# Performance work log

Measured on AMD Instinct MI355X. Metric: run time of the kernel, lower is better.

The kernel has to match this reference:

```python
import jax, jax.numpy as jnp
import numpy as np

N = 50000        # nodes
E_RAND = 800000  # random edges (avg degree 16)
F_IN = 512       # num_features
H = 128          # h_dim * num_heads = 16 * 8
C = 40           # num_classes
NEG_SLOPE = 0.2  # GATv2 default


def _glorot(key, shape):
    lim = float(np.sqrt(6.0 / (shape[0] + shape[1])))
    return jax.random.uniform(key, shape, jnp.float32, -lim, lim)


def setup_inputs() -> dict:
    key = jax.random.key(0)
    ks = jax.random.split(key, 12)
    src = jax.random.randint(ks[0], (E_RAND,), 0, N)
    dst = jax.random.randint(ks[1], (E_RAND,), 0, N)
    loop = jnp.arange(N)  # self-loops (GATv2Conv add_self_loops=True)
    edge_index = jnp.stack([jnp.concatenate([src, loop]),
                            jnp.concatenate([dst, loop])]).astype(jnp.int32)
    x = jax.random.normal(ks[2], (N, F_IN), jnp.float32)
    return {
        "x": x,
        "edge_index": edge_index,
        "W1l": _glorot(ks[3], (F_IN, H)), "b1l": jnp.zeros((H,), jnp.float32),
        "W1r": _glorot(ks[4], (F_IN, H)), "b1r": jnp.zeros((H,), jnp.float32),
        "a1": _glorot(ks[5], (H, 1)).reshape(H),
        "bias1": jnp.zeros((H,), jnp.float32),
        "W2l": _glorot(ks[6], (H, C)), "b2l": jnp.zeros((C,), jnp.float32),
        "W2r": _glorot(ks[7], (H, C)), "b2r": jnp.zeros((C,), jnp.float32),
        "a2": _glorot(ks[8], (C, 1)).reshape(C),
        "bias2": jnp.zeros((C,), jnp.float32),
    }


def gatv2_layer(x, src, dst, Wl, bl, Wr, br, att, bias, n):
    # PyG GATv2Conv, heads=1: xl = lin_l(x) (source side), xr = lin_r(x) (target side)
    xl = x @ Wl + bl                                   # [N, C_out]
    xr = x @ Wr + br                                   # [N, C_out]
    # edge score e_ij = a^T LeakyReLU(xl[j] + xr[i])
    e = jax.nn.leaky_relu(xl[src] + xr[dst], negative_slope=NEG_SLOPE) @ att  # [E]
    # segment softmax over edges grouped by destination node
    m = jax.ops.segment_max(e, dst, num_segments=n)    # every node has a self-loop
    ex = jnp.exp(e - m[dst])
    den = jax.ops.segment_sum(ex, dst, num_segments=n)
    alpha = ex / den[dst]                              # [E]
    # weighted scatter-aggregate of source-transformed features
    out = jax.ops.segment_sum(alpha[:, None] * xl[src], dst, num_segments=n)
    return out + bias


def reference(x, edge_index, W1l, b1l, W1r, b1r, a1, bias1,
              W2l, b2l, W2r, b2r, a2, bias2):
    # eval mode: dropout(p=0.6) is identity
    src, dst = edge_index[0], edge_index[1]
    n = x.shape[0]
    h = gatv2_layer(x, src, dst, W1l, b1l, W1r, b1r, a1, bias1, n)
    h = jax.nn.elu(h)
    h = gatv2_layer(h, src, dst, W2l, b2l, W2r, b2r, a2, bias2, n)
    return (h, jax.nn.log_softmax(h, axis=1))
```

## Files before the change

kernel.cpp:

```cpp
#include <hip/hip_runtime.h>
#include <math.h>

#define FIN 512
#define H1 128
#define C2 40
#define C2P 64

typedef __attribute__((ext_vector_type(8))) short short8;
typedef __attribute__((ext_vector_type(4))) float f32x4;

__device__ __forceinline__ ushort f2bf(float f) {
    union { float f; unsigned u; } c; c.f = f;
    unsigned u = c.u;
    return (ushort)((u + 0x7fffu + ((u >> 16) & 1u)) >> 16);
}
__device__ __forceinline__ float bf2f_lo(unsigned u) { return __uint_as_float(u << 16); }
__device__ __forceinline__ float bf2f_hi(unsigned u) { return __uint_as_float(u & 0xffff0000u); }

__global__ void count_k(const int* __restrict__ dst, int* __restrict__ cnt, int E) {
    int e = blockIdx.x * 256 + threadIdx.x;
    if (e < E) atomicAdd(&cnt[dst[e] + 1], 1);
}

__global__ __launch_bounds__(1024) void scan_k(int* __restrict__ arr, int ntot) {
    __shared__ int part[1024];
    int t = threadIdx.x;
    int chunk = (((ntot + 1023) / 1024) + 3) & ~3;
    int b = t * chunk;
    int s = 0;
    bool full = (b + chunk <= ntot);
    if (full) {
#pragma unroll 4
        for (int j = 0; j < chunk; j += 4) {
            int4 v = *reinterpret_cast<const int4*>(&arr[b + j]);
            s += v.x + v.y + v.z + v.w;
        }
    } else {
        for (int j = b; j < ntot; j++) s += arr[j];
    }
    part[t] = s;
    __syncthreads();
    for (int off = 1; off < 1024; off <<= 1) {
        int v = (t >= off) ? part[t - off] : 0;
        __syncthreads();
        part[t] += v;
        __syncthreads();
    }
    int run = (t == 0) ? 0 : part[t - 1];
    if (full) {
        for (int j = 0; j < chunk; j += 4) {
            int4 v = *reinterpret_cast<const int4*>(&arr[b + j]);
            int r0 = run + v.x, r1 = r0 + v.y, r2 = r1 + v.z, r3 = r2 + v.w;
            *reinterpret_cast<int4*>(&arr[b + j]) = make_int4(r0, r1, r2, r3);
            run = r3;
        }
    } else {
        for (int j = b; j < ntot; j++) { run += arr[j]; arr[j] = run; }
    }
}

__global__ void fill_k(const int* __restrict__ src, const int* __restrict__ dst,
                       const int* __restrict__ rowptr, int* __restrict__ fillp,
                       int* __restrict__ csr, int E) {
    int e = blockIdx.x * 256 + threadIdx.x;
    if (e < E) {
        int d = dst[e];
        int p = atomicAdd(&fillp[d], 1);
        csr[rowptr[d] + p] = src[e];
    }
}

__global__ void prep_k(const float* __restrict__ W1l, const float* __restrict__ W1r,
                       ushort* __restrict__ Wt2) {
    int idx = blockIdx.x * 256 + threadIdx.x;
    int kc  = idx >> 11;
    int rem = idx & 2047;
    int col = rem >> 3;
    int j   = rem & 7;
    int k   = kc * 8 + j;
    float v = (col < H1) ? W1l[k * H1 + col] : W1r[k * H1 + (col - H1)];
    Wt2[idx] = f2bf(v);
}

__global__ void prep2_k(const float* __restrict__ W2l, const float* __restrict__ W2r,
                        ushort* __restrict__ Ws) {
    int idx = blockIdx.x * 256 + threadIdx.x;
    if (idx >= 80 * H1) return;
    int col = idx >> 7;
    int k   = idx & 127;
    float v = (col < C2) ? W2l[k * C2 + col] : W2r[k * C2 + (col - C2)];
    Ws[idx] = f2bf(v);
}

__global__ __launch_bounds__(256) void gemm1_k(
    const float* __restrict__ x, const ushort* __restrict__ Wt2,
    const float* __restrict__ bl, const float* __restrict__ br,
    ushort* __restrict__ xlb, float* __restrict__ xr, int n)
{
    __shared__ ushort As[64][40];
    __shared__ ushort Bs[256][36];

    const int tid = threadIdx.x;
    const int r0  = blockIdx.x * 64;
    const int w    = tid >> 6;
    const int lane = tid & 63;
    const int l15  = lane & 15;
    const int lhi  = lane >> 4;

    f32x4 acc[4][4];
#pragma unroll
    for (int m = 0; m < 4; m++)
#pragma unroll
        for (int nn = 0; nn < 4; nn++) acc[m][nn] = (f32x4){0.f, 0.f, 0.f, 0.f};

    const int arow = tid >> 2;
    const int akc  = (tid & 3) * 8;
    const int arow_g = min(r0 + arow, n - 1);
    const float* aptr = x + (size_t)arow_g * FIN + akc;

    for (int kk = 0; kk < FIN; kk += 32) {
        float4 v0 = *reinterpret_cast<const float4*>(aptr + kk);
        float4 v1 = *reinterpret_cast<const float4*>(aptr + kk + 4);
        short8 ah;
        ah[0] = (short)f2bf(v0.x); ah[1] = (short)f2bf(v0.y);
        ah[2] = (short)f2bf(v0.z); ah[3] = (short)f2bf(v0.w);
        ah[4] = (short)f2bf(v1.x); ah[5] = (short)f2bf(v1.y);
        ah[6] = (short)f2bf(v1.z); ah[7] = (short)f2bf(v1.w);
        *reinterpret_cast<short8*>(&As[arow][akc]) = ah;

        int kc0 = kk >> 3;
#pragma unroll
        for (int q = 0; q < 4; q++) {
            short8 bh = *reinterpret_cast<const short8*>(&Wt2[(size_t)((kc0 + q) * 256 + tid) * 8]);
            *reinterpret_cast<short8*>(&Bs[tid][q * 8]) = bh;
        }
        __syncthreads();

        short8 af[4], bfr[4];
#pragma unroll
        for (int m = 0; m < 4; m++)
            af[m] = *reinterpret_cast<const short8*>(&As[m * 16 + l15][lhi * 8]);
#pragma unroll
        for (int nn = 0; nn < 4; nn++)
            bfr[nn] = *reinterpret_cast<const short8*>(&Bs[w * 64 + nn * 16 + l15][lhi * 8]);
#pragma unroll
        for (int m = 0; m < 4; m++)
#pragma unroll
            for (int nn = 0; nn < 4; nn++)
                acc[m][nn] = __builtin_amdgcn_mfma_f32_16x16x32_bf16(af[m], bfr[nn], acc[m][nn], 0, 0, 0);
        __syncthreads();
    }

#pragma unroll
    for (int nn = 0; nn < 4; nn++) {
        int col = w * 64 + nn * 16 + l15;
        bool left = (col < H1);
        float bias = left ? bl[col] : br[col - H1];
#pragma unroll
        for (int m = 0; m < 4; m++) {
#pragma unroll
            for (int r = 0; r < 4; r++) {
                int row = r0 + m * 16 + lhi * 4 + r;
                if (row < n) {
                    float v = acc[m][nn][r] + bias;
                    if (left) xlb[(size_t)row * H1 + col] = f2bf(v);
                    else      xr [(size_t)row * H1 + (col - H1)] = v;
                }
            }
        }
    }
}

__global__ __launch_bounds__(256) void edge1_k(
    const ushort* __restrict__ xlb, const float* xr,
    const int* __restrict__ rowptr, const int* __restrict__ csr,
    const float* __restrict__ att, const float* __restrict__ bias,
    float* h, int n)
{
    int wid  = threadIdx.x >> 6;
    int lane = threadIdx.x & 63;
    int grp  = lane >> 4;
    int gl   = lane & 15;
    int i = blockIdx.x * 4 + wid;
    if (i >= n) return;

    const float* xrp = &xr[(size_t)i * H1 + gl * 8];
    float4 xr0 = *reinterpret_cast<const float4*>(xrp);
    float4 xr1v = *reinterpret_cast<const float4*>(xrp + 4);
    float xrv[8] = {xr0.x, xr0.y, xr0.z, xr0.w, xr1v.x, xr1v.y, xr1v.z, xr1v.w};
    float4 a0 = *reinterpret_cast<const float4*>(&att[gl * 8]);
    float4 a1 = *reinterpret_cast<const float4*>(&att[gl * 8 + 4]);
    float av[8] = {a0.x, a0.y, a0.z, a0.w, a1.x, a1.y, a1.z, a1.w};

    int e0 = rowptr[i], e1 = rowptr[i + 1];

    float m = -INFINITY, den = 0.f;
    float acc[8];
#pragma unroll
    for (int f = 0; f < 8; f++) acc[f] = 0.f;

    int e = e0 + grp;
    uint4 u;
    if (e < e1) {
        int s = csr[e];
        u = *reinterpret_cast<const uint4*>(&xlb[(size_t)s * H1 + gl * 8]);
    }
    while (e < e1) {
        uint4 cu = u;
        int en = e + 4;
        if (en < e1) {
            int s2 = csr[en];
            u = *reinterpret_cast<const uint4*>(&xlb[(size_t)s2 * H1 + gl * 8]);
        }
        float xlv[8];
        xlv[0] = bf2f_lo(cu.x); xlv[1] = bf2f_hi(cu.x);
        xlv[2] = bf2f_lo(cu.y); xlv[3] = bf2f_hi(cu.y);
        xlv[4] = bf2f_lo(cu.z); xlv[5] = bf2f_hi(cu.z);
        xlv[6] = bf2f_lo(cu.w); xlv[7] = bf2f_hi(cu.w);
        float p = 0.f;
#pragma unroll
        for (int f = 0; f < 8; f++) {
            float t = xlv[f] + xrv[f];
            t = t > 0.f ? t : 0.2f * t;
            p += t * av[f];
        }
#pragma unroll
        for (int o = 8; o > 0; o >>= 1) p += __shfl_xor(p, o);
        float mn = fmaxf(m, p);
        float sc = __expf(m - mn);
        float wgt = __expf(p - mn);
        den = den * sc + wgt;
#pragma unroll
        for (int f = 0; f < 8; f++) acc[f] = acc[f] * sc + wgt * xlv[f];
        m = mn;
        e = en;
    }

    float mstar = m;
    mstar = fmaxf(mstar, __shfl_xor(mstar, 16));
    mstar = fmaxf(mstar, __shfl_xor(mstar, 32));
    float scale = __expf(m - mstar);
    den *= scale;
#pragma unroll
    for (int f = 0; f < 8; f++) acc[f] *= scale;
    den += __shfl_xor(den, 16); den += __shfl_xor(den, 32);
#pragma unroll
    for (int f = 0; f < 8; f++) {
        acc[f] += __shfl_xor(acc[f], 16);
        acc[f] += __shfl_xor(acc[f], 32);
    }

    if (grp == 0) {
        float inv = 1.f / den;
        float o[8];
#pragma unroll
        for (int f = 0; f < 8; f++) {
            float v = acc[f] * inv + bias[gl * 8 + f];
            o[f] = v > 0.f ? v : expm1f(v);
        }
        float* hp = &h[(size_t)i * H1 + gl * 8];
        *reinterpret_cast<float4*>(hp)     = make_float4(o[0], o[1], o[2], o[3]);
        *reinterpret_cast<float4*>(hp + 4) = make_float4(o[4], o[5], o[6], o[7]);
    }
}

__global__ __launch_bounds__(256) void gemm2_k(
    const float* __restrict__ h, const ushort* __restrict__ Ws,
    const float* __restrict__ bl, const float* __restrict__ br,
    ushort* __restrict__ xl2b, float* __restrict__ xr2, int n)
{
    __shared__ ushort WsL[80][136];

    const int tid = threadIdx.x;
    const int w    = tid >> 6;
    const int lane = tid & 63;
    const int l15  = lane & 15;
    const int lhi  = lane >> 4;
    const int r0 = blockIdx.x * 64;

#pragma unroll
    for (int q = 0; q < 5; q++) {
        int c = tid + q * 256;
        int col = c >> 4;
        int k0  = (c & 15) * 8;
        *reinterpret_cast<short8*>(&WsL[col][k0]) =
            *reinterpret_cast<const short8*>(&Ws[col * H1 + k0]);
    }
    __syncthreads();

    const int arow = min(r0 + w * 16 + l15, n - 1);
    const float* ap = &h[(size_t)arow * H1 + lhi * 8];

    f32x4 acc[5];
#pragma unroll
    for (int nt = 0; nt < 5; nt++) acc[nt] = (f32x4){0.f, 0.f, 0.f, 0.f};

#pragma unroll
    for (int kc = 0; kc < 4; kc++) {
        float4 v0 = *reinterpret_cast<const float4*>(ap + kc * 32);
        float4 v1 = *reinterpret_cast<const float4*>(ap + kc * 32 + 4);
        short8 af;
        af[0] = (short)f2bf(v0.x); af[1] = (short)f2bf(v0.y);
        af[2] = (short)f2bf(v0.z); af[3] = (short)f2bf(v0.w);
        af[4] = (short)f2bf(v1.x); af[5] = (short)f2bf(v1.y);
        af[6] = (short)f2bf(v1.z); af[7] = (short)f2bf(v1.w);
#pragma unroll
        for (int nt = 0; nt < 5; nt++) {
            short8 bf = *reinterpret_cast<const short8*>(&WsL[nt * 16 + l15][kc * 32 + lhi * 8]);
            acc[nt] = __builtin_amdgcn_mfma_f32_16x16x32_bf16(af, bf, acc[nt], 0, 0, 0);
        }
    }

#pragma unroll
    for (int nt = 0; nt < 5; nt++) {
        int col = nt * 16 + l15;
        float bias = (col < C2) ? bl[col] : br[col - C2];
#pragma unroll
        for (int r = 0; r < 4; r++) {
            int row = r0 + w * 16 + lhi * 4 + r;
            if (row < n) {
                float v = acc[nt][r] + bias;
                if (col < C2) xl2b[(size_t)row * C2P + col] = f2bf(v);
                else          xr2 [(size_t)row * C2  + (col - C2)] = v;
            }
        }
    }
    {
        int row = r0 + w * 16 + l15;
        int part = lhi;
        if (part < 3 && row < n) {
            uint4 z = make_uint4(0u, 0u, 0u, 0u);
            *reinterpret_cast<uint4*>(&xl2b[(size_t)row * C2P + C2 + part * 8]) = z;
        }
    }
}

__global__ __launch_bounds__(256) void edge2_k(
    const ushort* __restrict__ xl2b, const float* __restrict__ xr2,
    const int* __restrict__ rowptr, const int* __restrict__ csr,
    const float* __restrict__ att, const float* __restrict__ bias,
    float* __restrict__ out, int n)
{
    int wid  = threadIdx.x >> 6;
    int lane = threadIdx.x & 63;
    int grp  = lane >> 3;
    int gl   = lane & 7;
    int i = blockIdx.x * 4 + wid;
    if (i >= n) return;

    float xrv[8], av[8];
#pragma unroll
    for (int f = 0; f < 8; f++) {
        int idx = gl * 8 + f;
        bool real = idx < C2;
        xrv[f] = real ? xr2[(size_t)i * C2 + idx] : 0.f;
        av[f]  = real ? att[idx] : 0.f;
    }

    int e0 = rowptr[i], e1 = rowptr[i + 1];

    float m = -INFINITY, den = 0.f;
    float acc[8];
#pragma unroll
    for (int f = 0; f < 8; f++) acc[f] = 0.f;

    int e = e0 + grp;
    uint4 u;
    if (e < e1) {
        int s = csr[e];
        u = *reinterpret_cast<const uint4*>(&xl2b[(size_t)s * C2P + gl * 8]);
    }
    while (e < e1) {
        uint4 cu = u;
        int en = e + 8;
        if (en < e1) {
            int s2 = csr[en];
            u = *reinterpret_cast<const uint4*>(&xl2b[(size_t)s2 * C2P + gl * 8]);
        }
        float xlv[8];
        xlv[0] = bf2f_lo(cu.x); xlv[1] = bf2f_hi(cu.x);
        xlv[2] = bf2f_lo(cu.y); xlv[3] = bf2f_hi(cu.y);
        xlv[4] = bf2f_lo(cu.z); xlv[5] = bf2f_hi(cu.z);
        xlv[6] = bf2f_lo(cu.w); xlv[7] = bf2f_hi(cu.w);
        float p = 0.f;
#pragma unroll
        for (int f = 0; f < 8; f++) {
            float t = xlv[f] + xrv[f];
            t = t > 0.f ? t : 0.2f * t;
            p += t * av[f];
        }
#pragma unroll
        for (int o = 4; o > 0; o >>= 1) p += __shfl_xor(p, o);
        float mn = fmaxf(m, p);
        float sc = __expf(m - mn);
        float wgt = __expf(p - mn);
        den = den * sc + wgt;
#pragma unroll
        for (int f = 0; f < 8; f++) acc[f] = acc[f] * sc + wgt * xlv[f];
        m = mn;
        e = en;
    }

    float mstar = m;
    mstar = fmaxf(mstar, __shfl_xor(mstar, 8));
    mstar = fmaxf(mstar, __shfl_xor(mstar, 16));
    mstar = fmaxf(mstar, __shfl_xor(mstar, 32));
    float scale = __expf(m - mstar);
    den *= scale;
#pragma unroll
    for (int f = 0; f < 8; f++) acc[f] *= scale;
    den += __shfl_xor(den, 8); den += __shfl_xor(den, 16); den += __shfl_xor(den, 32);
#pragma unroll
    for (int f = 0; f < 8; f++) {
        acc[f] += __shfl_xor(acc[f], 8);
        acc[f] += __shfl_xor(acc[f], 16);
        acc[f] += __shfl_xor(acc[f], 32);
    }

    float inv = 1.f / den;
    bool real_lane = gl < 5;
    float o[8];
#pragma unroll
    for (int f = 0; f < 8; f++) {
        int idx = gl * 8 + f;
        o[f] = acc[f] * inv + (idx < C2 ? bias[idx] : 0.f);
    }

    float mv = -INFINITY;
    if (real_lane) {
#pragma unroll
        for (int f = 0; f < 8; f++) mv = fmaxf(mv, o[f]);
    }
    mv = fmaxf(mv, __shfl_xor(mv, 1));
    mv = fmaxf(mv, __shfl_xor(mv, 2));
    mv = fmaxf(mv, __shfl_xor(mv, 4));
    float se = 0.f;
    if (real_lane) {
#pragma unroll
        for (int f = 0; f < 8; f++) se += __expf(o[f] - mv);
    }
    se += __shfl_xor(se, 1); se += __shfl_xor(se, 2); se += __shfl_xor(se, 4);
    float lse = mv + logf(se);

    if (grp == 0 && real_lane) {
        float* op = &out[(size_t)i * C2 + gl * 8];
        *reinterpret_cast<float4*>(op)     = make_float4(o[0], o[1], o[2], o[3]);
        *reinterpret_cast<float4*>(op + 4) = make_float4(o[4], o[5], o[6], o[7]);
        float* lp = &out[(size_t)n * C2 + (size_t)i * C2 + gl * 8];
        *reinterpret_cast<float4*>(lp)     = make_float4(o[0] - lse, o[1] - lse, o[2] - lse, o[3] - lse);
        *reinterpret_cast<float4*>(lp + 4) = make_float4(o[4] - lse, o[5] - lse, o[6] - lse, o[7] - lse);
    }
}

extern "C" void kernel_launch(void* const* d_in, const int* in_sizes, int n_in,
                              void* d_out, int out_size, void* d_ws, size_t ws_size,
                              hipStream_t stream) {
    const float* x    = (const float*)d_in[0];
    const int*   ei   = (const int*)  d_in[1];
    const float* W1l  = (const float*)d_in[2];
    const float* b1l  = (const float*)d_in[3];
    const float* W1r  = (const float*)d_in[4];
    const float* b1r  = (const float*)d_in[5];
    const float* a1   = (const float*)d_in[6];
    const float* bias1= (const float*)d_in[7];
    const float* W2l  = (const float*)d_in[8];
    const float* b2l  = (const float*)d_in[9];
    const float* W2r  = (const float*)d_in[10];
    const float* b2r  = (const float*)d_in[11];
    const float* a2   = (const float*)d_in[12];
    const float* bias2= (const float*)d_in[13];

    const int N = in_sizes[0] / FIN;
    const int E = in_sizes[1] / 2;
    const int* src = ei;
    const int* dst = ei + E;

    float*  xr1 = (float*)d_ws;
    float*  xr2 = xr1 + (size_t)N * H1;
    ushort* xlb = (ushort*)(xr2 + (size_t)N * C2);
    ushort* xl2b = xlb;
    ushort* Wt2 = xlb + (size_t)N * H1;
    ushort* Ws2 = Wt2 + 131072;
    int* rowptr = (int*)(Ws2 + 10240);
    int* fillp  = rowptr + (N + 1);
    int* csr    = fillp + N;

    hipMemsetAsync(rowptr, 0, sizeof(int) * (size_t)(2 * N + 1), stream);
    count_k<<<(E + 255) / 256, 256, 0, stream>>>(dst, rowptr, E);
    scan_k<<<1, 1024, 0, stream>>>(rowptr, N + 1);
    fill_k<<<(E + 255) / 256, 256, 0, stream>>>(src, dst, rowptr, fillp, csr, E);

    prep_k<<<512, 256, 0, stream>>>(W1l, W1r, Wt2);
    prep2_k<<<40, 256, 0, stream>>>(W2l, W2r, Ws2);
    gemm1_k<<<(N + 63) / 64, 256, 0, stream>>>(x, Wt2, b1l, b1r, xlb, xr1, N);
    edge1_k<<<(N + 3) / 4, 256, 0, stream>>>(xlb, xr1, rowptr, csr, a1, bias1, xr1, N);
    gemm2_k<<<(N + 63) / 64, 256, 0, stream>>>(xr1, Ws2, b2l, b2r, xl2b, xr2, N);
    edge2_k<<<(N + 3) / 4, 256, 0, stream>>>(xl2b, xr2, rowptr, csr, a2, bias2, (float*)d_out, N);
}
```

Baseline: 296.4 us.

## Load MFMA fragments directly from global memory in gemm1, dropping LDS staging

gemm1 no longer stages A and B tiles through shared memory with two barriers per k-step. Each wave now loads its bf16 weight fragments and fp32 x rows straight into registers in MFMA layout. Launch bounds are raised to ask for 3 blocks per SM, and the manual bf16 rounding is swapped for the HIP intrinsic conversion in both GEMMs. The cost is redundant global/L2 reads: every wave reloads all four A row-tiles, and the weight fragments are loaded per wave.

```diff
diff --git a/kernel.cpp b/kernel.cpp
--- a/kernel.cpp
+++ b/kernel.cpp
@@ -1,4 +1,5 @@
 #include <hip/hip_runtime.h>
+#include <hip/hip_bf16.h>
 #include <math.h>
 
 #define FIN 512
@@ -16,6 +17,11 @@
 }
 __device__ __forceinline__ float bf2f_lo(unsigned u) { return __uint_as_float(u << 16); }
 __device__ __forceinline__ float bf2f_hi(unsigned u) { return __uint_as_float(u & 0xffff0000u); }
+
+__device__ __forceinline__ short bfc(float f) {
+    __hip_bfloat16 h = __float2bfloat16(f);
+    return *reinterpret_cast<short*>(&h);
+}
 
 __global__ void count_k(const int* __restrict__ dst, int* __restrict__ cnt, int E) {
     int e = blockIdx.x * 256 + threadIdx.x;
@@ -92,20 +98,17 @@
     Ws[idx] = f2bf(v);
 }
 
-__global__ __launch_bounds__(256) void gemm1_k(
+__global__ __launch_bounds__(256, 3) void gemm1_k(
     const float* __restrict__ x, const ushort* __restrict__ Wt2,
     const float* __restrict__ bl, const float* __restrict__ br,
     ushort* __restrict__ xlb, float* __restrict__ xr, int n)
 {
-    __shared__ ushort As[64][40];
-    __shared__ ushort Bs[256][36];
-
-    const int tid = threadIdx.x;
-    const int r0  = blockIdx.x * 64;
+    const int tid  = threadIdx.x;
     const int w    = tid >> 6;
     const int lane = tid & 63;
     const int l15  = lane & 15;
     const int lhi  = lane >> 4;
+    const int r0   = blockIdx.x * 64;
 
     f32x4 acc[4][4];
 #pragma unroll
@@ -113,42 +116,36 @@
 #pragma unroll
         for (int nn = 0; nn < 4; nn++) acc[m][nn] = (f32x4){0.f, 0.f, 0.f, 0.f};
 
-    const int arow = tid >> 2;
-    const int akc  = (tid & 3) * 8;
-    const int arow_g = min(r0 + arow, n - 1);
-    const float* aptr = x + (size_t)arow_g * FIN + akc;
-
+    const float* ap[4];
+#pragma unroll
+    for (int m = 0; m < 4; m++) {
+        int row = min(r0 + m * 16 + l15, n - 1);
+        ap[m] = x + (size_t)row * FIN + lhi * 8;
+    }
+    const ushort* bp = Wt2 + ((size_t)lhi * 256 + w * 64 + l15) * 8;
+
+#pragma unroll 2
     for (int kk = 0; kk < FIN; kk += 32) {
-        float4 v0 = *reinterpret_cast<const float4*>(aptr + kk);
-        float4 v1 = *reinterpret_cast<const float4*>(aptr + kk + 4);
-        short8 ah;
-        ah[0] = (short)f2bf(v0.x); ah[1] = (short)f2bf(v0.y);
-        ah[2] = (short)f2bf(v0.z); ah[3] = (short)f2bf(v0.w);
-        ah[4] = (short)f2bf(v1.x); ah[5] = (short)f2bf(v1.y);
-        ah[6] = (short)f2bf(v1.z); ah[7] = (short)f2bf(v1.w);
-        *reinterpret_cast<short8*>(&As[arow][akc]) = ah;
-
-        int kc0 = kk >> 3;
-#pragma unroll
-        for (int q = 0; q < 4; q++) {
-            short8 bh = *reinterpret_cast<const short8*>(&Wt2[(size_t)((kc0 + q) * 256 + tid) * 8]);
-            *reinterpret_cast<short8*>(&Bs[tid][q * 8]) = bh;
-        }
-        __syncthreads();
-
-        short8 af[4], bfr[4];
+        short8 bfrag[4];
+#pragma unroll
+        for (int nn = 0; nn < 4; nn++)
+            bfrag[nn] = *reinterpret_cast<const short8*>(bp + (size_t)(kk >> 3) * 2048 + nn * 128);
+
+        short8 afrag[4];
+#pragma unroll
+        for (int m = 0; m < 4; m++) {
+            float4 v0 = *reinterpret_cast<const float4*>(ap[m] + kk);
+            float4 v1 = *reinterpret_cast<const float4*>(ap[m] + kk + 4);
+            afrag[m][0] = bfc(v0.x); afrag[m][1] = bfc(v0.y);
+            afrag[m][2] = bfc(v0.z); afrag[m][3] = bfc(v0.w);
+            afrag[m][4] = bfc(v1.x); afrag[m][5] = bfc(v1.y);
+            afrag[m][6] = bfc(v1.z); afrag[m][7] = bfc(v1.w);
+        }
 #pragma unroll
         for (int m = 0; m < 4; m++)
-            af[m] = *reinterpret_cast<const short8*>(&As[m * 16 + l15][lhi * 8]);
-#pragma unroll
-        for (int nn = 0; nn < 4; nn++)
-            bfr[nn] = *reinterpret_cast<const short8*>(&Bs[w * 64 + nn * 16 + l15][lhi * 8]);
-#pragma unroll
-        for (int m = 0; m < 4; m++)
 #pragma unroll
             for (int nn = 0; nn < 4; nn++)
-                acc[m][nn] = __builtin_amdgcn_mfma_f32_16x16x32_bf16(af[m], bfr[nn], acc[m][nn], 0, 0, 0);
-        __syncthreads();
+                acc[m][nn] = __builtin_amdgcn_mfma_f32_16x16x32_bf16(afrag[m], bfrag[nn], acc[m][nn], 0, 0, 0);
     }
 
 #pragma unroll
@@ -300,10 +297,10 @@
         float4 v0 = *reinterpret_cast<const float4*>(ap + kc * 32);
         float4 v1 = *reinterpret_cast<const float4*>(ap + kc * 32 + 4);
         short8 af;
-        af[0] = (short)f2bf(v0.x); af[1] = (short)f2bf(v0.y);
-        af[2] = (short)f2bf(v0.z); af[3] = (short)f2bf(v0.w);
-        af[4] = (short)f2bf(v1.x); af[5] = (short)f2bf(v1.y);
-        af[6] = (short)f2bf(v1.z); af[7] = (short)f2bf(v1.w);
+        af[0] = bfc(v0.x); af[1] = bfc(v0.y);
+        af[2] = bfc(v0.z); af[3] = bfc(v0.w);
+        af[4] = bfc(v1.x); af[5] = bfc(v1.y);
+        af[6] = bfc(v1.z); af[7] = bfc(v1.w);
 #pragma unroll
         for (int nt = 0; nt < 5; nt++) {
             short8 bf = *reinterpret_cast<const short8*>(&WsL[nt * 16 + l15][kc * 32 + lhi * 8]);
```

Measured after the change: 321.0 us. 8.3% more time.
